# Optimization experiments

Hardware: AMD Instinct MI355X
Metric: run time of the kernel (lower is better)

Reference implementation:

```python
import jax, jax.numpy as jnp
import numpy as np

B = 8192      # batch
D = 512       # ode state dim = 4*h_dim
U = 100       # ode net hidden units
K_STEPS = 20  # opt.ode1_step
EPS = 0.01    # opt.ode2_eps


def setup_inputs() -> dict:
    key = jax.random.key(0)
    ks = jax.random.split(key, 12)
    std = 0.1  # init_network_weights std
    return {
        "y0": jax.random.normal(ks[0], (B, D), jnp.float32),
        "t_seq": jax.random.uniform(ks[1], (B, 2), dtype=jnp.float32),
        "W1": std * jax.random.normal(ks[2], (U, D), jnp.float32),
        "b1": jnp.zeros((U,), jnp.float32),
        "W2": std * jax.random.normal(ks[3], (U, U), jnp.float32),
        "b2": jnp.zeros((U,), jnp.float32),
        "W3": std * jax.random.normal(ks[4], (D, U), jnp.float32),
        "b3": jnp.zeros((D,), jnp.float32),
        "b_phi_zt": jax.random.normal(ks[5], (B, 1), jnp.float32),
        # derivative of Nonpositive net is <= 0; log(-b' + 0.01) requires b' < 0.01
        "b_phi_zt_deriv": -jax.random.uniform(ks[6], (B, 1), dtype=jnp.float32),
        "s_phi_zt": jax.random.normal(ks[7], (B, 1), jnp.float32),
        "s_phi_zt_deriv": jax.random.uniform(ks[8], (B, 1), dtype=jnp.float32),
        "k": K_STEPS,
    }


def _ode_net(y, W1, b1, W2, b2, W3, b3):
    # create_net(D, D, n_layers=1, n_units=U): Linear->Tanh->Linear->Tanh->Linear
    h = jnp.tanh(y @ W1.T + b1)
    h = jnp.tanh(h @ W2.T + b2)
    return h @ W3.T + b3


def _forward(y0, t_seq, W1, b1, W2, b2, W3, b3,
             b_phi_zt, b_phi_zt_deriv, s_phi_zt, s_phi_zt_deriv, k):
    # ---- DiffeqSolver: k fixed Euler steps, gradient net ignores t ----
    dt = (t_seq[:, 1:2] - t_seq[:, 0:1]) / k  # [B,1]

    def euler_step(yi, _):
        yi = yi + _ode_net(yi, W1, b1, W2, b2, W3, b3) * dt
        return yi, None

    y_final, _ = jax.lax.scan(euler_step, y0, None, length=k)

    # ---- DiffeqSolver_KL: y_t = y0 + eps * cumsum(g(m_t)); y0 = 0 ----
    const = 0.01
    Kv = s_phi_zt + jnp.log(-b_phi_zt_deriv + const) - jnp.log(s_phi_zt_deriv + const)  # [B,1]
    T = int(round(1.0 / EPS)) - 1  # steps t = 1 .. int(1/eps)-1
    ms = (-1.0 + EPS * jnp.arange(1, T + 1, dtype=jnp.float32))[:, None, None]  # [T,1,1]
    log_neg_m = jnp.log(-ms)
    gm = -b_phi_zt_deriv / (ms * log_neg_m) * (Kv - jnp.log(-log_neg_m))  # [T,B,1]
    ycum = EPS * jnp.cumsum(gm, axis=0)  # solutions[t-1] = ycum[t-1]
    loss = ycum[-1] + (ycum[-2] - ycum[-1])  # first_item + Gm_eps  -> [B,1]

    return jnp.concatenate([y_final, loss], axis=-1)  # [B, D+1]


def reference(y0, t_seq, W1, b1, W2, b2, W3, b3,
              b_phi_zt, b_phi_zt_deriv, s_phi_zt, s_phi_zt_deriv, k):
    return _forward(y0, t_seq, W1, b1, W2, b2, W3, b3,
                    b_phi_zt, b_phi_zt_deriv, s_phi_zt, s_phi_zt_deriv, k)
```

## Files before the change

### kernel.cpp

```cpp
#include <hip/hip_runtime.h>


typedef __attribute__((ext_vector_type(8))) short s16x8;
typedef __attribute__((ext_vector_type(4))) float fx4;

#define NB 8192
#define DD 512
#define UU 100
#define UP 128

__device__ __forceinline__ unsigned int f2bf(float x) {
  unsigned int u = __float_as_uint(x);
  return (u + 0x7FFFu + ((u >> 16) & 1u)) >> 16;
}
__device__ __forceinline__ float bf2f(unsigned int h) {
  return __uint_as_float(h << 16);
}
__device__ __forceinline__ unsigned int cvt_pk_bf16(float lo, float hi) {
  unsigned int r;
  asm("v_cvt_pk_bf16_f32 %0, %1, %2" : "=v"(r) : "v"(lo), "v"(hi));
  return r;
}
__device__ __forceinline__ float tanh5(float x) {
  float e = __builtin_amdgcn_exp2f(x * 2.885390081777927f);
  return 1.0f - 2.0f / (e + 1.0f);
}

__global__ void prep_weights(const float* __restrict__ W1,
                             const float* __restrict__ W2,
                             const float* __restrict__ W3,
                             const float* __restrict__ b2,
                             const float* __restrict__ b3,
                             unsigned short* __restrict__ ws) {
  int e = blockIdx.x * 256 + threadIdx.x;
  if (e < 65536) {
    int u = e >> 9, kc = e & 511;
    ws[e] = (u < UU) ? (unsigned short)f2bf(W1[u * DD + kc]) : (unsigned short)0;
  } else if (e < 81920) {
    int e2 = e - 65536;
    int n = e2 >> 7, kc = e2 & 127;
    unsigned short v = 0;
    if (kc == 127)      v = (n < UU) ? (unsigned short)f2bf(b2[n]) : (unsigned short)0;
    else if (n < UU && kc < UU) v = (unsigned short)f2bf(W2[n * UU + kc]);
    ws[e] = v;
  } else if (e < 147456) {
    int e3 = e - 81920;
    int d = e3 >> 7, kc = e3 & 127;
    unsigned short v = 0;
    if (kc == 127)      v = (unsigned short)f2bf(b3[d]);
    else if (kc < UU)   v = (unsigned short)f2bf(W3[d * UU + kc]);
    ws[e] = v;
  }
}

__global__ __launch_bounds__(512) __attribute__((amdgpu_waves_per_eu(2, 2)))
void ode_main(
    const float* __restrict__ y0, const float* __restrict__ t_seq,
    const float* __restrict__ b1,
    const unsigned short* __restrict__ W1b,
    const unsigned short* __restrict__ W2b,
    const unsigned short* __restrict__ W3b,
    const int* __restrict__ kptr, float* __restrict__ out) {
  __shared__ char Yb[32 * DD * 2];
  __shared__ char H1[32 * UP * 2];
  __shared__ char H2[32 * UP * 2];

  const int tid  = threadIdx.x;
  const int w    = tid >> 6;
  const int lane = tid & 63;
  const int lo   = lane & 15;
  const int hi   = lane >> 4;
  const int wb   = w - 4;
  const int b0   = blockIdx.x * 32;
  const int k    = *kptr;
  const float kinv = 1.0f / (float)k;

  auto ybo = [](int b, int byr) -> int { return (b << 10) + (byr ^ ((b & 7) << 4)); };
  auto ho  = [](int b, int byr) -> int { return (b << 8)  + (byr ^ ((b & 7) << 4)); };

  s16x8 wr[32];
  float b1v[2][4];
  if (w < 4) {
#pragma unroll
    for (int i = 0; i < 2; ++i)
#pragma unroll
      for (int kk = 0; kk < 16; ++kk)
        wr[i * 16 + kk] =
            *(const s16x8*)(W1b + ((2 * w + i) * 16 + lo) * DD + kk * 32 + hi * 8);
#pragma unroll
    for (int i = 0; i < 2; ++i)
#pragma unroll
      for (int r = 0; r < 4; ++r) {
        int u = (2 * w + i) * 16 + hi * 4 + r;
        b1v[i][r] = (u < UU) ? b1[u] : 0.0f;
      }
  } else {
#pragma unroll
    for (int i = 0; i < 8; ++i)
#pragma unroll
      for (int kk = 0; kk < 4; ++kk)
        wr[i * 4 + kk] =
            *(const s16x8*)(W3b + ((wb * 8 + i) * 16 + lo) * UP + kk * 32 + hi * 8);
  }
  s16x8 w2r[4];
#pragma unroll
  for (int kk = 0; kk < 4; ++kk)
    w2r[kk] = *(const s16x8*)(W2b + (w * 16 + lo) * UP + kk * 32 + hi * 8);
  float dt2[2];
#pragma unroll
  for (int j = 0; j < 2; ++j) {
    int b = b0 + j * 16 + lo;
    dt2[j] = (t_seq[2 * b + 1] - t_seq[2 * b]) * kinv;
  }

  fx4 Yr[8][2];
  if (w >= 4) {
#pragma unroll
    for (int i = 0; i < 8; ++i)
#pragma unroll
      for (int j = 0; j < 2; ++j) {
        const float* p =
            y0 + (size_t)(b0 + j * 16 + lo) * DD + (wb * 8 + i) * 16 + hi * 4;
        Yr[i][j] = *(const fx4*)p;
      }
  }

  auto write_yb = [&]() {
#pragma unroll
    for (int i = 0; i < 8; ++i)
#pragma unroll
      for (int j = 0; j < 2; ++j) {
        uint2 q;
        q.x = cvt_pk_bf16(Yr[i][j][0], Yr[i][j][1]);
        q.y = cvt_pk_bf16(Yr[i][j][2], Yr[i][j][3]);
        *(uint2*)(Yb + ybo(j * 16 + lo, ((wb * 8 + i) * 16 + hi * 4) * 2)) = q;
      }
  };
  if (w >= 4) write_yb();
  __syncthreads();

  const fx4 zf = {0.f, 0.f, 0.f, 0.f};

#pragma unroll 1
  for (int s = 0; s < k; ++s) {
    if (w < 4) {
      fx4 acc[2][2];
#pragma unroll
      for (int i = 0; i < 2; ++i)
#pragma unroll
        for (int j = 0; j < 2; ++j)
#pragma unroll
          for (int r = 0; r < 4; ++r) acc[i][j][r] = b1v[i][r];
      __builtin_amdgcn_s_setprio(1);
#pragma unroll
      for (int kk = 0; kk < 16; ++kk) {
        int bro = kk * 64 + hi * 16;
        s16x8 bb0 = *(const s16x8*)(Yb + ybo(lo, bro));
        s16x8 bb1 = *(const s16x8*)(Yb + ybo(16 + lo, bro));
        acc[0][0] = __builtin_amdgcn_mfma_f32_16x16x32_bf16(wr[kk], bb0, acc[0][0], 0, 0, 0);
        acc[0][1] = __builtin_amdgcn_mfma_f32_16x16x32_bf16(wr[kk], bb1, acc[0][1], 0, 0, 0);
        acc[1][0] = __builtin_amdgcn_mfma_f32_16x16x32_bf16(wr[16 + kk], bb0, acc[1][0], 0, 0, 0);
        acc[1][1] = __builtin_amdgcn_mfma_f32_16x16x32_bf16(wr[16 + kk], bb1, acc[1][1], 0, 0, 0);
      }
      __builtin_amdgcn_s_setprio(0);
#pragma unroll
      for (int i = 0; i < 2; ++i)
#pragma unroll
        for (int j = 0; j < 2; ++j) {
          float v0 = tanh5(acc[i][j][0]);
          float v1 = tanh5(acc[i][j][1]);
          float v2 = tanh5(acc[i][j][2]);
          float v3 = tanh5(acc[i][j][3]);
          if (w == 3 && i == 1 && hi == 3) v3 = 1.0f;
          uint2 q;
          q.x = cvt_pk_bf16(v0, v1);
          q.y = cvt_pk_bf16(v2, v3);
          *(uint2*)(H1 + ho(j * 16 + lo, ((2 * w + i) * 16 + hi * 4) * 2)) = q;
        }
    }
    __syncthreads();

    {
      fx4 c2[2];
      c2[0] = zf; c2[1] = zf;
      __builtin_amdgcn_s_setprio(1);
#pragma unroll
      for (int kk = 0; kk < 4; ++kk) {
        int bro = kk * 64 + hi * 16;
        s16x8 hb0 = *(const s16x8*)(H1 + ho(lo, bro));
        s16x8 hb1 = *(const s16x8*)(H1 + ho(16 + lo, bro));
        c2[0] = __builtin_amdgcn_mfma_f32_16x16x32_bf16(w2r[kk], hb0, c2[0], 0, 0, 0);
        c2[1] = __builtin_amdgcn_mfma_f32_16x16x32_bf16(w2r[kk], hb1, c2[1], 0, 0, 0);
      }
      __builtin_amdgcn_s_setprio(0);
#pragma unroll
      for (int j = 0; j < 2; ++j) {
        float h0 = tanh5(c2[j][0]) * dt2[j];
        float h1x = tanh5(c2[j][1]) * dt2[j];
        float h2x = tanh5(c2[j][2]) * dt2[j];
        float h3 = tanh5(c2[j][3]) * dt2[j];
        if (w == 7 && hi == 3) h3 = dt2[j];
        uint2 q;
        q.x = cvt_pk_bf16(h0, h1x);
        q.y = cvt_pk_bf16(h2x, h3);
        *(uint2*)(H2 + ho(j * 16 + lo, (w * 16 + hi * 4) * 2)) = q;
      }
    }
    __syncthreads();

    if (w >= 4) {
      __builtin_amdgcn_s_setprio(1);
#pragma unroll
      for (int kk = 0; kk < 4; ++kk) {
        int bro = kk * 64 + hi * 16;
        s16x8 bb0 = *(const s16x8*)(H2 + ho(lo, bro));
        s16x8 bb1 = *(const s16x8*)(H2 + ho(16 + lo, bro));
#pragma unroll
        for (int i = 0; i < 8; ++i) {
          Yr[i][0] = __builtin_amdgcn_mfma_f32_16x16x32_bf16(wr[i * 4 + kk], bb0, Yr[i][0], 0, 0, 0);
          Yr[i][1] = __builtin_amdgcn_mfma_f32_16x16x32_bf16(wr[i * 4 + kk], bb1, Yr[i][1], 0, 0, 0);
        }
      }
      __builtin_amdgcn_s_setprio(0);
      write_yb();
    }
    __syncthreads();
  }

  for (int idx = tid; idx < 32 * DD; idx += 512) {
    int b = idx >> 9, d = idx & 511;
    unsigned short hx = *(const unsigned short*)(Yb + ybo(b, 2 * d));
    out[(size_t)(b0 + b) * 513 + d] = bf2f((unsigned int)hx);
  }
}

__global__ void loss_kernel(const float* __restrict__ bdp,
                            const float* __restrict__ sp,
                            const float* __restrict__ sdp,
                            float* __restrict__ out) {
  int b = blockIdx.x * 256 + threadIdx.x;
  if (b >= NB) return;
  float bd = bdp[b];
  float Kv = sp[b] + __logf(-bd + 0.01f) - __logf(sdp[b] + 0.01f);
  float acc = 0.0f;
  for (int t = 1; t <= 98; ++t) {
    float m = 0.01f * (float)t - 1.0f;
    float L = __logf(-m);
    acc += (-bd) / (m * L) * (Kv - __logf(-L));
  }
  out[(size_t)b * 513 + 512] = 0.01f * acc;
}

extern "C" void kernel_launch(void* const* d_in, const int* in_sizes, int n_in,
                              void* d_out, int out_size, void* d_ws, size_t ws_size,
                              hipStream_t stream) {
  const float* y0    = (const float*)d_in[0];
  const float* t_seq = (const float*)d_in[1];
  const float* W1    = (const float*)d_in[2];
  const float* b1    = (const float*)d_in[3];
  const float* W2    = (const float*)d_in[4];
  const float* b2    = (const float*)d_in[5];
  const float* W3    = (const float*)d_in[6];
  const float* b3    = (const float*)d_in[7];
  const float* bd    = (const float*)d_in[9];
  const float* s_    = (const float*)d_in[10];
  const float* sd    = (const float*)d_in[11];
  const int*   kptr  = (const int*)d_in[12];
  float* out = (float*)d_out;
  unsigned short* ws = (unsigned short*)d_ws;

  prep_weights<<<576, 256, 0, stream>>>(W1, W2, W3, b2, b3, ws);
  ode_main<<<256, 512, 0, stream>>>(y0, t_seq, b1,
                                    ws, ws + 65536, ws + 81920, kptr, out);
  loss_kernel<<<32, 256, 0, stream>>>(bd, s_, sd, out);
}
```

Baseline: 112.1 us.

## Spread layer-1 and layer-3 MFMA work across all eight waves

Previously waves 0-3 did the W1 GEMM and waves 4-7 did the W3 GEMM, so half the waves sat idle in each phase. Now every wave computes 16 hidden units of layer 1 and 64 output columns of layer 3, holding W1, W2 and W3 fragments in registers at the same time. Layer 1 is also split into two independent accumulator chains to shorten MFMA dependency stalls. The cost is higher register pressure, since each wave now keeps all three weight sets plus the Y state.

```diff
diff --git a/kernel.cpp b/kernel.cpp
--- a/kernel.cpp
+++ b/kernel.cpp
@@ -8,6 +8,7 @@
 #define DD 512
 #define UU 100
 #define UP 128
+#define BM 32
 
 __device__ __forceinline__ unsigned int f2bf(float x) {
   unsigned int u = __float_as_uint(x);
@@ -61,51 +62,43 @@
     const unsigned short* __restrict__ W2b,
     const unsigned short* __restrict__ W3b,
     const int* __restrict__ kptr, float* __restrict__ out) {
-  __shared__ char Yb[32 * DD * 2];
-  __shared__ char H1[32 * UP * 2];
-  __shared__ char H2[32 * UP * 2];
+  __shared__ char Yb[BM * DD * 2];
+  __shared__ char H1[BM * UP * 2];
+  __shared__ char H2[BM * UP * 2];
 
   const int tid  = threadIdx.x;
   const int w    = tid >> 6;
   const int lane = tid & 63;
   const int lo   = lane & 15;
   const int hi   = lane >> 4;
-  const int wb   = w - 4;
-  const int b0   = blockIdx.x * 32;
+  const int b0   = blockIdx.x * BM;
   const int k    = *kptr;
   const float kinv = 1.0f / (float)k;
 
   auto ybo = [](int b, int byr) -> int { return (b << 10) + (byr ^ ((b & 7) << 4)); };
   auto ho  = [](int b, int byr) -> int { return (b << 8)  + (byr ^ ((b & 7) << 4)); };
 
-  s16x8 wr[32];
-  float b1v[2][4];
-  if (w < 4) {
-#pragma unroll
-    for (int i = 0; i < 2; ++i)
-#pragma unroll
-      for (int kk = 0; kk < 16; ++kk)
-        wr[i * 16 + kk] =
-            *(const s16x8*)(W1b + ((2 * w + i) * 16 + lo) * DD + kk * 32 + hi * 8);
-#pragma unroll
-    for (int i = 0; i < 2; ++i)
-#pragma unroll
-      for (int r = 0; r < 4; ++r) {
-        int u = (2 * w + i) * 16 + hi * 4 + r;
-        b1v[i][r] = (u < UU) ? b1[u] : 0.0f;
-      }
-  } else {
-#pragma unroll
-    for (int i = 0; i < 8; ++i)
-#pragma unroll
-      for (int kk = 0; kk < 4; ++kk)
-        wr[i * 4 + kk] =
-            *(const s16x8*)(W3b + ((wb * 8 + i) * 16 + lo) * UP + kk * 32 + hi * 8);
-  }
+  s16x8 w1r[16];
+#pragma unroll
+  for (int kk = 0; kk < 16; ++kk)
+    w1r[kk] = *(const s16x8*)(W1b + (16 * w + lo) * DD + kk * 32 + hi * 8);
   s16x8 w2r[4];
 #pragma unroll
   for (int kk = 0; kk < 4; ++kk)
-    w2r[kk] = *(const s16x8*)(W2b + (w * 16 + lo) * UP + kk * 32 + hi * 8);
+    w2r[kk] = *(const s16x8*)(W2b + (16 * w + lo) * UP + kk * 32 + hi * 8);
+  s16x8 w3r[4][4];
+#pragma unroll
+  for (int i = 0; i < 4; ++i)
+#pragma unroll
+    for (int kk = 0; kk < 4; ++kk)
+      w3r[i][kk] = *(const s16x8*)(W3b + ((4 * w + i) * 16 + lo) * UP + kk * 32 + hi * 8);
+
+  float b1v[4];
+#pragma unroll
+  for (int r = 0; r < 4; ++r) {
+    int u = 16 * w + 4 * hi + r;
+    b1v[r] = (u < UU) ? b1[u] : 0.0f;
+  }
   float dt2[2];
 #pragma unroll
   for (int j = 0; j < 2; ++j) {
@@ -113,70 +106,66 @@
     dt2[j] = (t_seq[2 * b + 1] - t_seq[2 * b]) * kinv;
   }
 
-  fx4 Yr[8][2];
-  if (w >= 4) {
-#pragma unroll
-    for (int i = 0; i < 8; ++i)
-#pragma unroll
-      for (int j = 0; j < 2; ++j) {
-        const float* p =
-            y0 + (size_t)(b0 + j * 16 + lo) * DD + (wb * 8 + i) * 16 + hi * 4;
-        Yr[i][j] = *(const fx4*)p;
-      }
-  }
+  fx4 Yr[4][2];
+#pragma unroll
+  for (int i = 0; i < 4; ++i)
+#pragma unroll
+    for (int j = 0; j < 2; ++j) {
+      const float* p = y0 + (size_t)(b0 + j * 16 + lo) * DD + (4 * w + i) * 16 + hi * 4;
+      Yr[i][j] = *(const fx4*)p;
+    }
 
   auto write_yb = [&]() {
 #pragma unroll
-    for (int i = 0; i < 8; ++i)
+    for (int i = 0; i < 4; ++i)
 #pragma unroll
       for (int j = 0; j < 2; ++j) {
         uint2 q;
         q.x = cvt_pk_bf16(Yr[i][j][0], Yr[i][j][1]);
         q.y = cvt_pk_bf16(Yr[i][j][2], Yr[i][j][3]);
-        *(uint2*)(Yb + ybo(j * 16 + lo, ((wb * 8 + i) * 16 + hi * 4) * 2)) = q;
+        *(uint2*)(Yb + ybo(j * 16 + lo, ((4 * w + i) * 16 + hi * 4) * 2)) = q;
       }
   };
-  if (w >= 4) write_yb();
+  write_yb();
   __syncthreads();
 
   const fx4 zf = {0.f, 0.f, 0.f, 0.f};
 
 #pragma unroll 1
   for (int s = 0; s < k; ++s) {
-    if (w < 4) {
-      fx4 acc[2][2];
-#pragma unroll
-      for (int i = 0; i < 2; ++i)
-#pragma unroll
-        for (int j = 0; j < 2; ++j)
-#pragma unroll
-          for (int r = 0; r < 4; ++r) acc[i][j][r] = b1v[i][r];
+    {
+      fx4 aA[2], aB[2];
+#pragma unroll
+      for (int j = 0; j < 2; ++j)
+#pragma unroll
+        for (int r = 0; r < 4; ++r) { aA[j][r] = b1v[r]; aB[j][r] = 0.0f; }
       __builtin_amdgcn_s_setprio(1);
 #pragma unroll
-      for (int kk = 0; kk < 16; ++kk) {
-        int bro = kk * 64 + hi * 16;
-        s16x8 bb0 = *(const s16x8*)(Yb + ybo(lo, bro));
-        s16x8 bb1 = *(const s16x8*)(Yb + ybo(16 + lo, bro));
-        acc[0][0] = __builtin_amdgcn_mfma_f32_16x16x32_bf16(wr[kk], bb0, acc[0][0], 0, 0, 0);
-        acc[0][1] = __builtin_amdgcn_mfma_f32_16x16x32_bf16(wr[kk], bb1, acc[0][1], 0, 0, 0);
-        acc[1][0] = __builtin_amdgcn_mfma_f32_16x16x32_bf16(wr[16 + kk], bb0, acc[1][0], 0, 0, 0);
-        acc[1][1] = __builtin_amdgcn_mfma_f32_16x16x32_bf16(wr[16 + kk], bb1, acc[1][1], 0, 0, 0);
+      for (int kk = 0; kk < 16; kk += 2) {
+        int bro0 = kk * 64 + hi * 16;
+        int bro1 = (kk + 1) * 64 + hi * 16;
+        s16x8 b00 = *(const s16x8*)(Yb + ybo(lo, bro0));
+        s16x8 b01 = *(const s16x8*)(Yb + ybo(16 + lo, bro0));
+        s16x8 b10 = *(const s16x8*)(Yb + ybo(lo, bro1));
+        s16x8 b11 = *(const s16x8*)(Yb + ybo(16 + lo, bro1));
+        aA[0] = __builtin_amdgcn_mfma_f32_16x16x32_bf16(w1r[kk], b00, aA[0], 0, 0, 0);
+        aA[1] = __builtin_amdgcn_mfma_f32_16x16x32_bf16(w1r[kk], b01, aA[1], 0, 0, 0);
+        aB[0] = __builtin_amdgcn_mfma_f32_16x16x32_bf16(w1r[kk + 1], b10, aB[0], 0, 0, 0);
+        aB[1] = __builtin_amdgcn_mfma_f32_16x16x32_bf16(w1r[kk + 1], b11, aB[1], 0, 0, 0);
       }
       __builtin_amdgcn_s_setprio(0);
 #pragma unroll
-      for (int i = 0; i < 2; ++i)
-#pragma unroll
-        for (int j = 0; j < 2; ++j) {
-          float v0 = tanh5(acc[i][j][0]);
-          float v1 = tanh5(acc[i][j][1]);
-          float v2 = tanh5(acc[i][j][2]);
-          float v3 = tanh5(acc[i][j][3]);
-          if (w == 3 && i == 1 && hi == 3) v3 = 1.0f;
-          uint2 q;
-          q.x = cvt_pk_bf16(v0, v1);
-          q.y = cvt_pk_bf16(v2, v3);
-          *(uint2*)(H1 + ho(j * 16 + lo, ((2 * w + i) * 16 + hi * 4) * 2)) = q;
-        }
+      for (int j = 0; j < 2; ++j) {
+        float v0 = tanh5(aA[j][0] + aB[j][0]);
+        float v1 = tanh5(aA[j][1] + aB[j][1]);
+        float v2 = tanh5(aA[j][2] + aB[j][2]);
+        float v3 = tanh5(aA[j][3] + aB[j][3]);
+        if (w == 7 && hi == 3) v3 = 1.0f;
+        uint2 q;
+        q.x = cvt_pk_bf16(v0, v1);
+        q.y = cvt_pk_bf16(v2, v3);
+        *(uint2*)(H1 + ho(j * 16 + lo, (16 * w + 4 * hi) * 2)) = q;
+      }
     }
     __syncthreads();
 
@@ -203,31 +192,29 @@
         uint2 q;
         q.x = cvt_pk_bf16(h0, h1x);
         q.y = cvt_pk_bf16(h2x, h3);
-        *(uint2*)(H2 + ho(j * 16 + lo, (w * 16 + hi * 4) * 2)) = q;
+        *(uint2*)(H2 + ho(j * 16 + lo, (16 * w + 4 * hi) * 2)) = q;
       }
     }
     __syncthreads();
 
-    if (w >= 4) {
-      __builtin_amdgcn_s_setprio(1);
-#pragma unroll
-      for (int kk = 0; kk < 4; ++kk) {
-        int bro = kk * 64 + hi * 16;
-        s16x8 bb0 = *(const s16x8*)(H2 + ho(lo, bro));
-        s16x8 bb1 = *(const s16x8*)(H2 + ho(16 + lo, bro));
-#pragma unroll
-        for (int i = 0; i < 8; ++i) {
-          Yr[i][0] = __builtin_amdgcn_mfma_f32_16x16x32_bf16(wr[i * 4 + kk], bb0, Yr[i][0], 0, 0, 0);
-          Yr[i][1] = __builtin_amdgcn_mfma_f32_16x16x32_bf16(wr[i * 4 + kk], bb1, Yr[i][1], 0, 0, 0);
-        }
-      }
-      __builtin_amdgcn_s_setprio(0);
-      write_yb();
-    }
+    __builtin_amdgcn_s_setprio(1);
+#pragma unroll
+    for (int kk = 0; kk < 4; ++kk) {
+      int bro = kk * 64 + hi * 16;
+      s16x8 bb0 = *(const s16x8*)(H2 + ho(lo, bro));
+      s16x8 bb1 = *(const s16x8*)(H2 + ho(16 + lo, bro));
+#pragma unroll
+      for (int i = 0; i < 4; ++i) {
+        Yr[i][0] = __builtin_amdgcn_mfma_f32_16x16x32_bf16(w3r[i][kk], bb0, Yr[i][0], 0, 0, 0);
+        Yr[i][1] = __builtin_amdgcn_mfma_f32_16x16x32_bf16(w3r[i][kk], bb1, Yr[i][1], 0, 0, 0);
+      }
+    }
+    __builtin_amdgcn_s_setprio(0);
+    write_yb();
     __syncthreads();
   }
 
-  for (int idx = tid; idx < 32 * DD; idx += 512) {
+  for (int idx = tid; idx < BM * DD; idx += 512) {
     int b = idx >> 9, d = idx & 511;
     unsigned short hx = *(const unsigned short*)(Yb + ybo(b, 2 * d));
     out[(size_t)(b0 + b) * 513 + d] = bf2f((unsigned int)hx);
```

New measurement: 94.26 us. 15.9% less time.
